# Optimization experiments

Hardware: AMD Instinct MI355X
Metric: run time of the kernel (lower is better)

The kernel has to match this reference:

```python
import jax, jax.numpy as jnp
import numpy as np

N, E, F_IN = 50000, 800000, 256
H, C = 4, 64            # heads, per-head channels; H*C == 256
OUT = 64
NEG_SLOPE = 0.2


def _gat_conv(x, src, dst, W, a_src, a_dst, b):
    """PyG-style GATConv (concat=True, add_self_loops already applied in src/dst)."""
    n = x.shape[0]
    h = (x @ W).reshape(n, H, C)                      # [N,H,C]
    al_s = jnp.sum(h * a_src, axis=-1)                # [N,H]
    al_d = jnp.sum(h * a_dst, axis=-1)                # [N,H]
    e = jax.nn.leaky_relu(al_s[src] + al_d[dst], NEG_SLOPE)   # [E,H]
    # segment softmax over incoming edges of each dst node
    emax = jax.ops.segment_max(e, dst, num_segments=n)
    ee = jnp.exp(e - emax[dst])
    denom = jax.ops.segment_sum(ee, dst, num_segments=n)
    alpha = ee / denom[dst]                           # [E,H]
    msg = alpha[:, :, None] * h[src]                  # [E,H,C]
    out = jax.ops.segment_sum(msg, dst, num_segments=n)
    return out.reshape(n, H * C) + b


def setup_inputs() -> dict:
    key = jax.random.key(0)
    ks = jax.random.split(key, 12)
    x = jax.random.normal(ks[0], (N, F_IN), dtype=jnp.float32)
    edge_index = jax.random.randint(ks[1], (2, E), 0, N, dtype=jnp.int64)
    batch = jnp.zeros((N,), dtype=jnp.int64)

    def glorot(k, shape):
        fan = shape[0]
        return jax.random.normal(k, shape, dtype=jnp.float32) / jnp.sqrt(jnp.float32(fan))

    params = {
        "W1": glorot(ks[2], (F_IN, H * C)),
        "a_src1": jax.random.normal(ks[3], (H, C), dtype=jnp.float32) * 0.1,
        "a_dst1": jax.random.normal(ks[4], (H, C), dtype=jnp.float32) * 0.1,
        "b1": jnp.zeros((H * C,), dtype=jnp.float32),
        "W2": glorot(ks[5], (H * C, H * C)),
        "a_src2": jax.random.normal(ks[6], (H, C), dtype=jnp.float32) * 0.1,
        "a_dst2": jax.random.normal(ks[7], (H, C), dtype=jnp.float32) * 0.1,
        "b2": jnp.zeros((H * C,), dtype=jnp.float32),
        "fcW": glorot(ks[8], (H * C, OUT)),
        "fcb": jnp.zeros((OUT,), dtype=jnp.float32),
    }
    return {"x": x, "edge_index": edge_index, "batch": batch, **params}


def reference(x, edge_index, batch, W1, a_src1, a_dst1, b1, W2, a_src2, a_dst2, b2, fcW, fcb):
    n = x.shape[0]
    # PyG GATConv default add_self_loops=True
    loop = jnp.arange(n, dtype=edge_index.dtype)
    src = jnp.concatenate([edge_index[0], loop])
    dst = jnp.concatenate([edge_index[1], loop])

    h = jax.nn.elu(_gat_conv(x, src, dst, W1, a_src1, a_dst1, b1))
    h = jax.nn.elu(_gat_conv(h, src, dst, W2, a_src2, a_dst2, b2))
    # dropout is identity in eval mode; node_level=True -> no pooling
    logits = h @ fcW + fcb
    return logits
```

## Files before the change

### kernel.cpp

```cpp
#include <hip/hip_runtime.h>
#include <hip/hip_bf16.h>


#define HEADS 4
#define FDIM  256

typedef __attribute__((ext_vector_type(4))) float f32x4;
typedef __attribute__((ext_vector_type(8))) short s16x8;

__device__ __forceinline__ void gload_lds16(const void* g, void* l) {
    __builtin_amdgcn_global_load_lds(
        (__attribute__((address_space(1))) void*)g,
        (__attribute__((address_space(3))) void*)l, 16, 0, 0);
}

__device__ __forceinline__ float b2f(unsigned short u) {
    return __uint_as_float((unsigned)u << 16);
}
__device__ __forceinline__ unsigned short f2b(float f) {
    __hip_bfloat16 b = __float2bfloat16(f);
    return *(unsigned short*)&b;
}

__device__ __forceinline__ float fast_exp2(float t) {
#if __has_builtin(__builtin_amdgcn_exp2f)
    return __builtin_amdgcn_exp2f(t);
#else
    return __expf(t * 0.6931471805599453f);
#endif
}

__global__ void cvt_all(const float* __restrict__ x, unsigned short* __restrict__ xb,
                        const float* __restrict__ W1, unsigned short* __restrict__ Wt1,
                        const float* __restrict__ W2, unsigned short* __restrict__ Wt2,
                        const float* __restrict__ fcW, unsigned short* __restrict__ fcWt,
                        const int* __restrict__ dstp, int* __restrict__ deg,
                        int nx, int E, int Et) {
    int i = blockIdx.x * 256 + threadIdx.x;
    if (i < nx) { xb[i] = f2b(x[i]); return; }
    i -= nx;
    if (i < FDIM * FDIM) {
        int r = i >> 8, c = i & 255;
        Wt1[c * FDIM + r] = f2b(W1[i]);
        return;
    }
    i -= FDIM * FDIM;
    if (i < FDIM * FDIM) {
        int r = i >> 8, c = i & 255;
        Wt2[c * FDIM + r] = f2b(W2[i]);
        return;
    }
    i -= FDIM * FDIM;
    if (i < FDIM * 64) {
        int r = i >> 6, c = i & 63;
        fcWt[c * FDIM + r] = f2b(fcW[i]);
        return;
    }
    i -= FDIM * 64;
    if (i < Et) {
        int dd = (i < E) ? dstp[i] : (i - E);
        atomicAdd(&deg[dd], 1);
    }
}

template <int BN, bool F32OUT, bool ATT, bool SCAT>
__global__ __launch_bounds__(256, 2)
void gemm_bt_k256(const unsigned short* __restrict__ A,
                  const unsigned short* __restrict__ Bt,
                  void* __restrict__ C,
                  const float* __restrict__ bias,
                  const float* __restrict__ a_src,
                  const float* __restrict__ a_dst,
                  float* __restrict__ als,
                  float* __restrict__ ald,
                  int M, int ncol,
                  const int* __restrict__ sc_src,
                  const int* __restrict__ sc_dst,
                  int* __restrict__ cursor,
                  int* __restrict__ csrs,
                  int E, int n) {
    constexpr int BM = 128, BK = 64;
    constexpr int NFRAG = BN / 32;
    __shared__ __align__(16) unsigned short lA[BM * BK];
    __shared__ __align__(16) unsigned short lB[BN * BK];

    if constexpr (SCAT) {
        const int mb = (M + 127) >> 7;
        if ((int)blockIdx.x >= mb) {
            const int sb = gridDim.x - mb;
            int e = (blockIdx.y * sb + ((int)blockIdx.x - mb)) * 256
                    + (int)threadIdx.x;
            const int Et = E + n;
            if (e < Et) {
                int s, dd;
                if (e < E) { s = sc_src[e]; dd = sc_dst[e]; }
                else       { s = e - E;     dd = s; }
                int p = atomicAdd(&cursor[dd], 1);
                csrs[p] = s;
            }
            return;
        }
    }

    const int tid  = threadIdx.x;
    const int lane = tid & 63;
    const int wave = tid >> 6;
    const int wm = wave & 1, wn = wave >> 1;
    const int m0 = blockIdx.x * BM;
    const int n0 = blockIdx.y * BN;
    const int quad = lane >> 4, col16 = lane & 15;

    f32x4 acc[4][NFRAG];
#pragma unroll
    for (int i = 0; i < 4; ++i)
#pragma unroll
        for (int j = 0; j < NFRAG; ++j) acc[i][j] = (f32x4){0.f, 0.f, 0.f, 0.f};

#pragma unroll 1
    for (int kt = 0; kt < 4; ++kt) {
        const int k0 = kt * BK;
#pragma unroll
        for (int i = 0; i < 4; ++i) {
            int slot = tid + i * 256;
            int row = slot >> 3, g = slot & 7;
            int gs = g ^ (row & 7);
            int rg = m0 + row; rg = rg < M ? rg : (M - 1);
            gload_lds16(A + (size_t)rg * FDIM + k0 + gs * 8,
                        (char*)lA + (size_t)slot * 16);
        }
#pragma unroll
        for (int i = 0; i < BN * 8 / 256; ++i) {
            int slot = tid + i * 256;
            int row = slot >> 3, g = slot & 7;
            int gs = g ^ (row & 7);
            gload_lds16(Bt + (size_t)(n0 + row) * FDIM + k0 + gs * 8,
                        (char*)lB + (size_t)slot * 16);
        }
        __syncthreads();

#pragma unroll
        for (int kk = 0; kk < 2; ++kk) {
            const int kg = kk * 4 + quad;
            s16x8 af[4], bfr[NFRAG];
#pragma unroll
            for (int i = 0; i < 4; ++i) {
                int row = wm * 64 + i * 16 + col16;
                int g = kg ^ (row & 7);
                af[i] = *(const s16x8*)((const char*)lA + (size_t)(row * 8 + g) * 16);
            }
#pragma unroll
            for (int j = 0; j < NFRAG; ++j) {
                int row = wn * (BN / 2) + j * 16 + col16;
                int g = kg ^ (row & 7);
                bfr[j] = *(const s16x8*)((const char*)lB + (size_t)(row * 8 + g) * 16);
            }
#pragma unroll
            for (int i = 0; i < 4; ++i)
#pragma unroll
                for (int j = 0; j < NFRAG; ++j)
                    acc[i][j] = __builtin_amdgcn_mfma_f32_16x16x32_bf16(
                        af[i], bfr[j], acc[i][j], 0, 0, 0);
        }
        __syncthreads();
    }

#pragma unroll
    for (int i = 0; i < 4; ++i) {
#pragma unroll
        for (int j = 0; j < NFRAG; ++j) {
#pragma unroll
            for (int r = 0; r < 4; ++r) {
                int row = m0 + wm * 64 + i * 16 + quad * 4 + r;
                int col = n0 + wn * (BN / 2) + j * 16 + col16;
                if (row < M) {
                    float v = acc[i][j][r];
                    if (bias) v += bias[col];
                    if constexpr (F32OUT)
                        ((float*)C)[(size_t)row * ncol + col] = v;
                    else
                        ((unsigned short*)C)[(size_t)row * ncol + col] = f2b(v);
                }
            }
        }
    }

    if constexpr (ATT) {
        constexpr float LOG2E = 1.4426950408889634f;
        const int head = blockIdx.y * 2 + wn;
        float asv[4], adv[4];
#pragma unroll
        for (int j = 0; j < 4; ++j) {
            int c = head * 64 + j * 16 + col16;
            asv[j] = a_src[c] * LOG2E;
            adv[j] = a_dst[c] * LOG2E;
        }
#pragma unroll
        for (int i = 0; i < 4; ++i) {
#pragma unroll
            for (int r = 0; r < 4; ++r) {
                float vs = acc[i][0][r] * asv[0] + acc[i][1][r] * asv[1]
                         + acc[i][2][r] * asv[2] + acc[i][3][r] * asv[3];
                float vd = acc[i][0][r] * adv[0] + acc[i][1][r] * adv[1]
                         + acc[i][2][r] * adv[2] + acc[i][3][r] * adv[3];
#pragma unroll
                for (int m = 1; m < 16; m <<= 1) {
                    vs += __shfl_xor(vs, m, 16);
                    vd += __shfl_xor(vd, m, 16);
                }
                int row = m0 + wm * 64 + i * 16 + quad * 4 + r;
                if (col16 == 0 && row < M) {
                    als[row * HEADS + head] = vs;
                    ald[row * HEADS + head] = vd;
                }
            }
        }
    }
}

__global__ void csr_scan(const int* __restrict__ deg, int* __restrict__ offs,
                         int* __restrict__ cursor, int n) {
    __shared__ int red[4];
    __shared__ int wsums[4];
    __shared__ int base_sh;
    const int tid = threadIdx.x, lane = tid & 63, wv = tid >> 6;
    const int start = blockIdx.x * 256;

    int base = 0;
    for (int i = tid * 4; i < start; i += 1024) {
        int4 v = *(const int4*)(deg + i);
        base += v.x + v.y + v.z + v.w;
    }
#pragma unroll
    for (int m = 1; m < 64; m <<= 1) base += __shfl_xor(base, m, 64);
    if (lane == 0) red[wv] = base;
    __syncthreads();
    if (tid == 0) base_sh = red[0] + red[1] + red[2] + red[3];

    const int i = start + tid;
    int v = (i < n) ? deg[i] : 0;
    int acc = v;
#pragma unroll
    for (int d = 1; d < 64; d <<= 1) {
        int t = __shfl_up(acc, d, 64);
        if (lane >= d) acc += t;
    }
    if (lane == 63) wsums[wv] = acc;
    __syncthreads();
    int wo = 0;
#pragma unroll
    for (int k = 0; k < 4; ++k) wo += (k < wv) ? wsums[k] : 0;
    if (i < n) {
        int o = base_sh + wo + acc - v;
        offs[i] = o;
        cursor[i] = o;
    }
}

__global__ void gat_gather(const int* __restrict__ off,
                           const int* __restrict__ deg,
                           const int* __restrict__ csr_src,
                           const float* __restrict__ als,
                           const float* __restrict__ ald,
                           const unsigned short* __restrict__ h,
                           const float* __restrict__ bias,
                           unsigned short* __restrict__ x2, int n) {
    const int lane = threadIdx.x & 63;
    const int d = (blockIdx.x * blockDim.x + threadIdx.x) >> 6;
    if (d >= n) return;
    const int head = lane >> 4;
    const float aldh = ald[4 * d + head];
    const int start = off[d];
    const int end = start + deg[d];

    float a0 = 0.f, a1 = 0.f, a2 = 0.f, a3 = 0.f, den = 0.f;
    int j = start;
    for (; j + 8 <= end; j += 8) {
        int s[8];
#pragma unroll
        for (int u = 0; u < 8; ++u) s[u] = csr_src[j + u];
        float e[8];
#pragma unroll
        for (int u = 0; u < 8; ++u) e[u] = als[4 * s[u] + head];
        ushort4 hv[8];
#pragma unroll
        for (int u = 0; u < 8; ++u)
            hv[u] = *(const ushort4*)(h + (size_t)s[u] * FDIM + lane * 4);
#pragma unroll
        for (int u = 0; u < 8; ++u) {
            float t = e[u] + aldh;
            t = t > 0.f ? t : 0.2f * t;
            float w = fast_exp2(t);
            den += w;
            a0 += w * b2f(hv[u].x);
            a1 += w * b2f(hv[u].y);
            a2 += w * b2f(hv[u].z);
            a3 += w * b2f(hv[u].w);
        }
    }
    for (; j + 4 <= end; j += 4) {
        int s[4];
#pragma unroll
        for (int u = 0; u < 4; ++u) s[u] = csr_src[j + u];
        float e[4];
#pragma unroll
        for (int u = 0; u < 4; ++u) e[u] = als[4 * s[u] + head];
        ushort4 hv[4];
#pragma unroll
        for (int u = 0; u < 4; ++u)
            hv[u] = *(const ushort4*)(h + (size_t)s[u] * FDIM + lane * 4);
#pragma unroll
        for (int u = 0; u < 4; ++u) {
            float t = e[u] + aldh;
            t = t > 0.f ? t : 0.2f * t;
            float w = fast_exp2(t);
            den += w;
            a0 += w * b2f(hv[u].x);
            a1 += w * b2f(hv[u].y);
            a2 += w * b2f(hv[u].z);
            a3 += w * b2f(hv[u].w);
        }
    }
    for (; j < end; ++j) {
        int s = csr_src[j];
        float t = als[4 * s + head] + aldh;
        t = t > 0.f ? t : 0.2f * t;
        float w = fast_exp2(t);
        ushort4 hv = *(const ushort4*)(h + (size_t)s * FDIM + lane * 4);
        den += w;
        a0 += w * b2f(hv.x);
        a1 += w * b2f(hv.y);
        a2 += w * b2f(hv.z);
        a3 += w * b2f(hv.w);
    }
    const float inv = 1.0f / den;
    const int c = lane * 4;
    float v0 = a0 * inv + bias[c + 0];
    float v1 = a1 * inv + bias[c + 1];
    float v2 = a2 * inv + bias[c + 2];
    float v3 = a3 * inv + bias[c + 3];
    v0 = v0 > 0.f ? v0 : expm1f(v0);
    v1 = v1 > 0.f ? v1 : expm1f(v1);
    v2 = v2 > 0.f ? v2 : expm1f(v2);
    v3 = v3 > 0.f ? v3 : expm1f(v3);
    ushort4 o;
    o.x = f2b(v0); o.y = f2b(v1); o.z = f2b(v2); o.w = f2b(v3);
    *(ushort4*)(x2 + (size_t)d * FDIM + c) = o;
}

extern "C" void kernel_launch(void* const* d_in, const int* in_sizes, int n_in,
                              void* d_out, int out_size, void* d_ws, size_t ws_size,
                              hipStream_t stream) {
    const float* x   = (const float*)d_in[0];
    const int*   ei  = (const int*)d_in[1];
    const float* W1  = (const float*)d_in[3];
    const float* as1 = (const float*)d_in[4];
    const float* ad1 = (const float*)d_in[5];
    const float* b1  = (const float*)d_in[6];
    const float* W2  = (const float*)d_in[7];
    const float* as2 = (const float*)d_in[8];
    const float* ad2 = (const float*)d_in[9];
    const float* b2  = (const float*)d_in[10];
    const float* fcW = (const float*)d_in[11];
    const float* fcb = (const float*)d_in[12];
    float* out = (float*)d_out;

    const int n = in_sizes[0] / FDIM;
    const int E = in_sizes[1] / 2;
    const int Etot = E + n;
    const int* srcp = ei;
    const int* dstp = ei + E;
    const int nb = (n + 255) / 256;

    char* ws = (char*)d_ws;
    size_t off_b = 0;
    auto carve = [&](size_t bytes) -> char* {
        char* p = ws + off_b;
        off_b += (bytes + 255) & ~(size_t)255;
        return p;
    };
    unsigned short* xb = (unsigned short*)carve((size_t)n * FDIM * 2);
    unsigned short* h  = (unsigned short*)carve((size_t)n * FDIM * 2);
    float* als  = (float*)carve((size_t)n * HEADS * 4);
    float* ald  = (float*)carve((size_t)n * HEADS * 4);
    int* deg    = (int*)carve((size_t)n * 4);
    int* offs   = (int*)carve((size_t)(n + 1) * 4);
    int* cursor = (int*)carve((size_t)n * 4);
    int* csr_src = (int*)carve((size_t)Etot * 4);
    unsigned short* Wt1  = (unsigned short*)carve(FDIM * FDIM * 2);
    unsigned short* Wt2  = (unsigned short*)carve(FDIM * FDIM * 2);
    unsigned short* fcWt = (unsigned short*)carve(64 * FDIM * 2);
    unsigned short* x2 = xb;

    const int mblocks = (n + 127) / 128;
    const int nx = n * FDIM;
    const int cvt_total = nx + 2 * FDIM * FDIM + FDIM * 64 + Etot;
    const int SB = (Etot + 511) / 512;

    hipMemsetAsync(deg, 0, (size_t)n * 4, stream);

    cvt_all<<<(cvt_total + 255) / 256, 256, 0, stream>>>(
        x, xb, W1, Wt1, W2, Wt2, fcW, fcWt, dstp, deg, nx, E, Etot);

    csr_scan<<<nb, 256, 0, stream>>>(deg, offs, cursor, n);

    gemm_bt_k256<128, false, true, true><<<dim3(mblocks + SB, 2), 256, 0, stream>>>(
        xb, Wt1, h, nullptr, as1, ad1, als, ald, n, FDIM,
        srcp, dstp, cursor, csr_src, E, n);
    gat_gather<<<(n + 3) / 4, 256, 0, stream>>>(
        offs, deg, csr_src, als, ald, h, b1, x2, n);

    gemm_bt_k256<128, false, true, false><<<dim3(mblocks, 2), 256, 0, stream>>>(
        x2, Wt2, h, nullptr, as2, ad2, als, ald, n, FDIM,
        nullptr, nullptr, nullptr, nullptr, 0, 0);
    gat_gather<<<(n + 3) / 4, 256, 0, stream>>>(
        offs, deg, csr_src, als, ald, h, b2, x2, n);

    gemm_bt_k256<64, true, false, false><<<dim3(mblocks, 1), 256, 0, stream>>>(
        x2, fcWt, out, fcb, nullptr, nullptr, nullptr, nullptr, n, 64,
        nullptr, nullptr, nullptr, nullptr, 0, 0);
}
```

Baseline: 378.9 us.

## Double-buffer GEMM LDS loads, remap blocks across XCDs, vectorize x conversion

The GEMM kernel now double-buffers its LDS tiles, prefetching the next K-slice with global_load_lds while MFMAs run on the current one, and waits with explicit vmcnt and s_barrier. The grid is flattened to 1D and block IDs are remapped so consecutive tiles (both N-halves of an M-tile) land on the same XCD, improving L2 reuse of A rows. The fp32-to-bf16 conversion of x is vectorized to float4 per thread. Doubling LDS use may lower occupancy, and the hand-written waitcnt depends on how many loads each thread issues.

```diff
diff --git a/kernel.cpp b/kernel.cpp
--- a/kernel.cpp
+++ b/kernel.cpp
@@ -35,10 +35,16 @@
                         const float* __restrict__ W2, unsigned short* __restrict__ Wt2,
                         const float* __restrict__ fcW, unsigned short* __restrict__ fcWt,
                         const int* __restrict__ dstp, int* __restrict__ deg,
-                        int nx, int E, int Et) {
+                        int nx4, int E, int Et) {
     int i = blockIdx.x * 256 + threadIdx.x;
-    if (i < nx) { xb[i] = f2b(x[i]); return; }
-    i -= nx;
+    if (i < nx4) {
+        float4 v = ((const float4*)x)[i];
+        ushort4 o;
+        o.x = f2b(v.x); o.y = f2b(v.y); o.z = f2b(v.z); o.w = f2b(v.w);
+        ((ushort4*)xb)[i] = o;
+        return;
+    }
+    i -= nx4;
     if (i < FDIM * FDIM) {
         int r = i >> 8, c = i & 255;
         Wt1[c * FDIM + r] = f2b(W1[i]);
@@ -81,15 +87,19 @@
                   int E, int n) {
     constexpr int BM = 128, BK = 64;
     constexpr int NFRAG = BN / 32;
-    __shared__ __align__(16) unsigned short lA[BM * BK];
-    __shared__ __align__(16) unsigned short lB[BN * BK];
+    constexpr int BOPS = BN * 8 / 256;
+    constexpr int SOPS = 4 + BOPS;
+    constexpr int YNUM = (BN == 128) ? 2 : 1;
+    __shared__ __align__(16) unsigned short lA[2][BM * BK];
+    __shared__ __align__(16) unsigned short lB[2][BN * BK];
+
+    const int mb = (M + 127) >> 7;
+    const int nwg = mb * YNUM;
+    int bid = blockIdx.x;
 
     if constexpr (SCAT) {
-        const int mb = (M + 127) >> 7;
-        if ((int)blockIdx.x >= mb) {
-            const int sb = gridDim.x - mb;
-            int e = (blockIdx.y * sb + ((int)blockIdx.x - mb)) * 256
-                    + (int)threadIdx.x;
+        if (bid >= nwg) {
+            int e = (bid - nwg) * 256 + (int)threadIdx.x;
             const int Et = E + n;
             if (e < Et) {
                 int s, dd;
@@ -102,12 +112,20 @@
         }
     }
 
+    {
+        const int q = nwg >> 3, r = nwg & 7;
+        const int xcd = bid & 7, sub = bid >> 3;
+        bid = (xcd < r ? xcd * (q + 1) : r * (q + 1) + (xcd - r) * q) + sub;
+    }
+    const int gy = (YNUM == 2) ? (bid & 1) : 0;
+    const int gx = (YNUM == 2) ? (bid >> 1) : bid;
+
     const int tid  = threadIdx.x;
     const int lane = tid & 63;
     const int wave = tid >> 6;
     const int wm = wave & 1, wn = wave >> 1;
-    const int m0 = blockIdx.x * BM;
-    const int n0 = blockIdx.y * BN;
+    const int m0 = gx * BM;
+    const int n0 = gy * BN;
     const int quad = lane >> 4, col16 = lane & 15;
 
     f32x4 acc[4][NFRAG];
@@ -116,8 +134,7 @@
 #pragma unroll
         for (int j = 0; j < NFRAG; ++j) acc[i][j] = (f32x4){0.f, 0.f, 0.f, 0.f};
 
-#pragma unroll 1
-    for (int kt = 0; kt < 4; ++kt) {
+    auto stage = [&](int kt, int buf) {
         const int k0 = kt * BK;
 #pragma unroll
         for (int i = 0; i < 4; ++i) {
@@ -126,17 +143,32 @@
             int gs = g ^ (row & 7);
             int rg = m0 + row; rg = rg < M ? rg : (M - 1);
             gload_lds16(A + (size_t)rg * FDIM + k0 + gs * 8,
-                        (char*)lA + (size_t)slot * 16);
-        }
-#pragma unroll
-        for (int i = 0; i < BN * 8 / 256; ++i) {
+                        (char*)lA[buf] + (size_t)slot * 16);
+        }
+#pragma unroll
+        for (int i = 0; i < BOPS; ++i) {
             int slot = tid + i * 256;
             int row = slot >> 3, g = slot & 7;
             int gs = g ^ (row & 7);
             gload_lds16(Bt + (size_t)(n0 + row) * FDIM + k0 + gs * 8,
-                        (char*)lB + (size_t)slot * 16);
-        }
-        __syncthreads();
+                        (char*)lB[buf] + (size_t)slot * 16);
+        }
+    };
+
+    stage(0, 0);
+
+#pragma unroll 1
+    for (int kt = 0; kt < 4; ++kt) {
+        const int cur = kt & 1;
+        if (kt < 3) {
+            stage(kt + 1, cur ^ 1);
+            asm volatile("s_waitcnt vmcnt(%0)" :: "i"(SOPS) : "memory");
+        } else {
+            asm volatile("s_waitcnt vmcnt(0)" ::: "memory");
+        }
+        __builtin_amdgcn_sched_barrier(0);
+        __builtin_amdgcn_s_barrier();
+        __builtin_amdgcn_sched_barrier(0);
 
 #pragma unroll
         for (int kk = 0; kk < 2; ++kk) {
@@ -146,13 +178,13 @@
             for (int i = 0; i < 4; ++i) {
                 int row = wm * 64 + i * 16 + col16;
                 int g = kg ^ (row & 7);
-                af[i] = *(const s16x8*)((const char*)lA + (size_t)(row * 8 + g) * 16);
+                af[i] = *(const s16x8*)((const char*)lA[cur] + (size_t)(row * 8 + g) * 16);
             }
 #pragma unroll
             for (int j = 0; j < NFRAG; ++j) {
                 int row = wn * (BN / 2) + j * 16 + col16;
                 int g = kg ^ (row & 7);
-                bfr[j] = *(const s16x8*)((const char*)lB + (size_t)(row * 8 + g) * 16);
+                bfr[j] = *(const s16x8*)((const char*)lB[cur] + (size_t)(row * 8 + g) * 16);
             }
 #pragma unroll
             for (int i = 0; i < 4; ++i)
@@ -161,7 +193,10 @@
                     acc[i][j] = __builtin_amdgcn_mfma_f32_16x16x32_bf16(
                         af[i], bfr[j], acc[i][j], 0, 0, 0);
         }
-        __syncthreads();
+
+        __builtin_amdgcn_sched_barrier(0);
+        __builtin_amdgcn_s_barrier();
+        __builtin_amdgcn_sched_barrier(0);
     }
 
 #pragma unroll
@@ -186,7 +221,7 @@
 
     if constexpr (ATT) {
         constexpr float LOG2E = 1.4426950408889634f;
-        const int head = blockIdx.y * 2 + wn;
+        const int head = gy * 2 + wn;
         float asv[4], adv[4];
 #pragma unroll
         for (int j = 0; j < 4; ++j) {
@@ -392,30 +427,30 @@
     unsigned short* x2 = xb;
 
     const int mblocks = (n + 127) / 128;
-    const int nx = n * FDIM;
-    const int cvt_total = nx + 2 * FDIM * FDIM + FDIM * 64 + Etot;
-    const int SB = (Etot + 511) / 512;
+    const int nx4 = n * FDIM / 4;
+    const int cvt_total = nx4 + 2 * FDIM * FDIM + FDIM * 64 + Etot;
+    const int SB = (Etot + 255) / 256;
 
     hipMemsetAsync(deg, 0, (size_t)n * 4, stream);
 
     cvt_all<<<(cvt_total + 255) / 256, 256, 0, stream>>>(
-        x, xb, W1, Wt1, W2, Wt2, fcW, fcWt, dstp, deg, nx, E, Etot);
+        x, xb, W1, Wt1, W2, Wt2, fcW, fcWt, dstp, deg, nx4, E, Etot);
 
     csr_scan<<<nb, 256, 0, stream>>>(deg, offs, cursor, n);
 
-    gemm_bt_k256<128, false, true, true><<<dim3(mblocks + SB, 2), 256, 0, stream>>>(
+    gemm_bt_k256<128, false, true, true><<<mblocks * 2 + SB, 256, 0, stream>>>(
         xb, Wt1, h, nullptr, as1, ad1, als, ald, n, FDIM,
         srcp, dstp, cursor, csr_src, E, n);
     gat_gather<<<(n + 3) / 4, 256, 0, stream>>>(
         offs, deg, csr_src, als, ald, h, b1, x2, n);
 
-    gemm_bt_k256<128, false, true, false><<<dim3(mblocks, 2), 256, 0, stream>>>(
+    gemm_bt_k256<128, false, true, false><<<mblocks * 2, 256, 0, stream>>>(
         x2, Wt2, h, nullptr, as2, ad2, als, ald, n, FDIM,
         nullptr, nullptr, nullptr, nullptr, 0, 0);
     gat_gather<<<(n + 3) / 4, 256, 0, stream>>>(
         offs, deg, csr_src, als, ald, h, b2, x2, n);
 
-    gemm_bt_k256<64, true, false, false><<<dim3(mblocks, 1), 256, 0, stream>>>(
+    gemm_bt_k256<64, true, false, false><<<mblocks, 256, 0, stream>>>(
         x2, fcWt, out, fcb, nullptr, nullptr, nullptr, nullptr, n, 64,
         nullptr, nullptr, nullptr, nullptr, 0, 0);
 }
```

Result: slower. 394.6 us (+4.1%).
